# Performance work log

Measured on AMD Instinct MI355X. Metric: run time of the kernel, lower is better.

Reference implementation:

```python
import jax, jax.numpy as jnp
import numpy as np

SCALING = 32.0 / 16.0  # lora_alpha / lora_rank


def setup_inputs() -> dict:
    key = jax.random.key(0)
    ks = jax.random.split(key, 6)
    B_, S, D, O, E, R = 4, 2048, 4096, 4096, 8, 16
    x = jax.random.normal(ks[0], (B_, S, D), dtype=jnp.float32)
    W_base = jax.random.normal(ks[1], (O, D), dtype=jnp.float32) * (D ** -0.5)
    b_base = jax.random.normal(ks[2], (O,), dtype=jnp.float32) * 0.01
    W_gate = jax.random.normal(ks[3], (E, D), dtype=jnp.float32) * (D ** -0.5)
    A = jax.random.normal(ks[4], (E, R, D), dtype=jnp.float32) * (D ** -0.5)
    B = jax.random.normal(ks[5], (O, R), dtype=jnp.float32)[None] * (R ** -0.5)
    B = jnp.broadcast_to(B, (E, O, R)) * jnp.linspace(0.5, 1.5, E)[:, None, None]
    return {"x": x, "W_base": W_base, "b_base": b_base, "W_gate": W_gate,
            "A": A, "B": B, "top_k": 2}


def reference(x, W_base, b_base, W_gate, A, B, top_k):
    D = x.shape[-1]
    O = W_base.shape[0]
    E = W_gate.shape[0]
    xf = x.reshape(-1, D)                      # [N, D] flattened tokens
    N = xf.shape[0]

    # base linear
    base = jnp.einsum('nd,od->no', xf, W_base) + b_base          # [N, O]

    # gating: softmax then top-k, renormalize selected weights
    gate_logits = jax.nn.softmax(xf @ W_gate.T, axis=-1)          # [N, E]
    w, sel = jax.lax.top_k(gate_logits, top_k)                    # [N, k]
    w = w / jnp.sum(w, axis=-1, keepdims=True)

    # dense per-(token, expert) weight; non-selected experts get 0,
    # equivalent to the scatter-add combine in the original code.
    w_dense = jnp.zeros((N, E), dtype=x.dtype).at[
        jnp.arange(N)[:, None], sel].set(w)                       # [N, E]

    # LoRA expert compute: down-proj for every expert (rank is small),
    # weight, then up-proj and combine across experts.
    h = jnp.einsum('nd,erd->ner', xf, A)                          # [N, E, R]
    hw = h * w_dense[:, :, None]                                  # [N, E, R]
    moe = jnp.einsum('ner,eor->no', hw, B) * SCALING              # [N, O]

    out = (base + moe).reshape(x.shape[:-1] + (O,))
    return out
```

## Files before the change

kernel.cpp:

```cpp
#include <hip/hip_runtime.h>
#include <stdint.h>

typedef unsigned short u16;
typedef float f32x4 __attribute__((ext_vector_type(4)));
typedef short bf16x8 __attribute__((ext_vector_type(8)));

static __device__ __forceinline__ u16 f2bf(float f) {
  union { float f; unsigned u; } a; a.f = f;
  unsigned r = a.u + 0x7fffu + ((a.u >> 16) & 1u);
  return (u16)(r >> 16);
}

static __device__ __forceinline__ void gld16(const void* g, void* l) {
  __builtin_amdgcn_global_load_lds(
      (const __attribute__((address_space(1))) void*)(uintptr_t)g,
      (__attribute__((address_space(3))) void*)(uintptr_t)l,
      16, 0, 0);
}

__global__ __launch_bounds__(256) void cast_strided(
    const float* __restrict__ src, u16* __restrict__ dst,
    int rows, int cols, int ldd) {
  const size_t total = (size_t)rows * cols / 4;
  for (size_t i = (size_t)blockIdx.x * 256 + threadIdx.x; i < total;
       i += (size_t)gridDim.x * 256) {
    const size_t e = i * 4;
    const int r = (int)(e / cols);
    const int c = (int)(e % cols);
    float4 v = *(const float4*)(src + e);
    ushort4 o;
    o.x = f2bf(v.x); o.y = f2bf(v.y); o.z = f2bf(v.z); o.w = f2bf(v.w);
    *(ushort4*)(dst + (size_t)r * ldd + c) = o;
  }
}

__global__ __launch_bounds__(256) void cast_b2(
    const float* __restrict__ B, u16* __restrict__ Waug) {
  int i = blockIdx.x * 256 + threadIdx.x;
  if (i >= 4096 * 128) return;
  const int o = i >> 7;
  const int er = i & 127;
  const int e = er >> 4;
  const int r = er & 15;
  float v = B[((size_t)e * 4096 + o) * 16 + r] * 2.0f;
  Waug[(size_t)o * 4224 + 4096 + er] = f2bf(v);
}

__global__ __launch_bounds__(256) void cast_x_gate(
    const float* __restrict__ x, const float* __restrict__ Wg,
    u16* __restrict__ Xaug, float* __restrict__ wsc) {
  const int lane = threadIdx.x & 63;
  const int wv = threadIdx.x >> 6;
  const int n = blockIdx.x * 4 + wv;
  const float4* x4 = (const float4*)(x + (size_t)n * 4096);
  const float4* g4 = (const float4*)Wg;
  u16* xr = Xaug + (size_t)n * 4224;
  float acc[8] = {0, 0, 0, 0, 0, 0, 0, 0};
#pragma unroll
  for (int ii = 0; ii < 16; ++ii) {
    const int i = ii * 64 + lane;
    float4 xv = x4[i];
    ushort4 o;
    o.x = f2bf(xv.x); o.y = f2bf(xv.y); o.z = f2bf(xv.z); o.w = f2bf(xv.w);
    *(ushort4*)(xr + i * 4) = o;
#pragma unroll
    for (int e = 0; e < 8; ++e) {
      float4 w4 = g4[e * 1024 + i];
      acc[e] += xv.x * w4.x + xv.y * w4.y + xv.z * w4.z + xv.w * w4.w;
    }
  }
#pragma unroll
  for (int e = 0; e < 8; ++e) {
#pragma unroll
    for (int off = 32; off > 0; off >>= 1)
      acc[e] += __shfl_xor(acc[e], off);
  }
  int i1 = 0; float m1 = acc[0];
#pragma unroll
  for (int e = 1; e < 8; ++e) if (acc[e] > m1) { m1 = acc[e]; i1 = e; }
  int i2 = -1; float m2 = -3.4e38f;
#pragma unroll
  for (int e = 0; e < 8; ++e) if (e != i1 && acc[e] > m2) { m2 = acc[e]; i2 = e; }
  float w1 = 1.0f / (1.0f + expf(m2 - m1));
  float w2 = 1.0f - w1;
  if (lane < 8)
    wsc[(size_t)n * 8 + lane] = (lane == i1) ? w1 : ((lane == i2) ? w2 : 0.0f);
}

__global__ __launch_bounds__(256) void lora_down(
    const u16* __restrict__ Xa, const u16* __restrict__ A2,
    float* __restrict__ hp) {
  __shared__ u16 sA[128 * 64];
  __shared__ u16 sB[128 * 64];
  const int t = threadIdx.x;
  const int lane = t & 63;
  const int wr = t >> 7;
  const int wc = (t >> 6) & 1;
  const int l15 = lane & 15;
  const int lhi = lane >> 4;
  f32x4 acc[4][4] = {};

  const int brow = blockIdx.x * 128;
  const int kbase = blockIdx.y * 1024;
  const int srow = t >> 3;
  const int scol = (t & 7) * 8;
  const size_t a_src = (size_t)(brow + srow) * 4224 + scol + kbase;
  const size_t b_src = (size_t)srow * 4096 + scol + kbase;

  for (int k0 = 0; k0 < 1024; k0 += 64) {
#pragma unroll
    for (int c = 0; c < 4; ++c)
      gld16(Xa + a_src + (size_t)c * 32 * 4224 + k0,
            &sA[(c * 32 + srow) * 64 + scol]);
#pragma unroll
    for (int c = 0; c < 4; ++c)
      gld16(A2 + b_src + (size_t)c * 32 * 4096 + k0,
            &sB[(c * 32 + srow) * 64 + scol]);
    __syncthreads();
#pragma unroll
    for (int kk = 0; kk < 2; ++kk) {
      bf16x8 av[4], bv[4];
#pragma unroll
      for (int m = 0; m < 4; ++m)
        av[m] = *(const bf16x8*)&sA[(wr * 64 + m * 16 + l15) * 64 + kk * 32 + lhi * 8];
#pragma unroll
      for (int n = 0; n < 4; ++n)
        bv[n] = *(const bf16x8*)&sB[(wc * 64 + n * 16 + l15) * 64 + kk * 32 + lhi * 8];
#pragma unroll
      for (int m = 0; m < 4; ++m)
#pragma unroll
        for (int n = 0; n < 4; ++n)
          acc[m][n] = __builtin_amdgcn_mfma_f32_16x16x32_bf16(av[m], bv[n], acc[m][n], 0, 0, 0);
    }
    __syncthreads();
  }
  float* out = hp + (size_t)blockIdx.y * (8192 * 128);
#pragma unroll
  for (int m = 0; m < 4; ++m) {
    const int rbase = brow + wr * 64 + m * 16 + lhi * 4;
#pragma unroll
    for (int n = 0; n < 4; ++n) {
      const int col = wc * 64 + n * 16 + l15;
#pragma unroll
      for (int j = 0; j < 4; ++j)
        out[(size_t)(rbase + j) * 128 + col] = acc[m][n][j];
    }
  }
}

__global__ __launch_bounds__(256) void reduce_hw(
    const float* __restrict__ hp, const float* __restrict__ wsc,
    u16* __restrict__ Xaug) {
  int i = blockIdx.x * 256 + threadIdx.x;
  if (i >= 8192 * 128) return;
  const int n = i >> 7;
  const int er = i & 127;
  const int e = er >> 4;
  float v = hp[i] + hp[i + 1048576] + hp[i + 2097152] + hp[i + 3145728];
  Xaug[(size_t)n * 4224 + 4096 + er] = f2bf(v * wsc[n * 8 + e]);
}

#define BAR do { asm volatile("" ::: "memory"); __builtin_amdgcn_s_barrier(); asm volatile("" ::: "memory"); } while (0)

#define RDA(BUF, MH)                                                            \
  { _Pragma("unroll") for (int mm = 0; mm < 4; ++mm)                            \
    _Pragma("unroll") for (int kk = 0; kk < 2; ++kk)                            \
      av[mm][kk] = *(const bf16x8*)(lds + (BUF) + fbA + ((((MH) * 4 + mm) * 2 + kk) << 10)); }

#define RDB(BUF, NH)                                                            \
  { _Pragma("unroll") for (int nn = 0; nn < 2; ++nn)                            \
    _Pragma("unroll") for (int kk = 0; kk < 2; ++kk)                            \
      bv[(NH) * 2 + nn][kk] = *(const bf16x8*)(lds + (BUF) + fbB + ((((NH) * 2 + nn) * 2 + kk) << 10)); }

#define MFMAQ(MH, NH)                                                           \
  { __builtin_amdgcn_s_setprio(1);                                              \
    _Pragma("unroll") for (int kk = 0; kk < 2; ++kk)                            \
    _Pragma("unroll") for (int mm = 0; mm < 4; ++mm)                            \
    _Pragma("unroll") for (int nn = 0; nn < 2; ++nn)                            \
      acc[(MH) * 4 + mm][(NH) * 2 + nn] = __builtin_amdgcn_mfma_f32_16x16x32_bf16( \
          av[mm][kk], bv[(NH) * 2 + nn][kk], acc[(MH) * 4 + mm][(NH) * 2 + nn], 0, 0, 0); \
    __builtin_amdgcn_s_setprio(0); }

__global__ __launch_bounds__(512, 2) void gemm8p(
    const u16* __restrict__ Ag, const u16* __restrict__ Bg,
    const float* __restrict__ bias, float* __restrict__ C,
    int lda, int ldb, int ldc, int K, int tiles_n) {
  __shared__ __align__(1024) char lds[131072];
  const int t = threadIdx.x;
  const int lane = t & 63;
  const int w = t >> 6;
  const int wr = w >> 2, wc = w & 3;
  const int l15 = lane & 15, lhi = lane >> 4;

  const int cpx = gridDim.x >> 3;
  const int bid = blockIdx.x;
  const int swz = (bid & 7) * cpx + (bid >> 3);
  const int tile_m = swz / tiles_n;
  const int tile_n = swz % tiles_n;
  const int brow = tile_m << 8;
  const int bcol = tile_n << 8;

  const int sb = (lane << 4) ^ (lane & 32);
  const int srow = sb >> 6;
  const int scol = (sb & 63) >> 1;

  const u16* pA[4]; const u16* pB[4];
#pragma unroll
  for (int s = 0; s < 4; ++s) {
    const int idx = w * 4 + s;
    const int rg = idx >> 1, cs = idx & 1;
    pA[s] = Ag + (size_t)(brow + rg * 16 + srow) * lda + cs * 32 + scol;
    pB[s] = Bg + (size_t)(bcol + rg * 16 + srow) * ldb + cs * 32 + scol;
  }
  const int ldsA = w << 12;
  const int ldsB = 32768 + (w << 12);

  const int innerL = ((l15 << 6) + (lhi << 4)) ^ ((l15 & 8) << 2);
  const int fbA = (wr << 14) + innerL;
  const int fbB = 32768 + (wc << 13) + innerL;

  f32x4 acc[8][4] = {};
  bf16x8 av[4][2], bv[4][2];

  const int NT = K >> 6;

#pragma unroll
  for (int s = 0; s < 4; ++s) gld16(pA[s], lds + ldsA + (s << 10));
#pragma unroll
  for (int s = 0; s < 4; ++s) gld16(pB[s], lds + ldsB + (s << 10));
#pragma unroll
  for (int s = 0; s < 4; ++s) gld16(pB[s] + 64, lds + 65536 + ldsB + (s << 10));
#pragma unroll
  for (int s = 0; s < 4; ++s) { pA[s] += 64; pB[s] += 128; }
  asm volatile("s_waitcnt vmcnt(4)" ::: "memory");
  BAR;
  RDA(0, 0); RDB(0, 0);

  for (int j = 0; j < NT; ++j) {
    const int buf  = (j & 1) << 16;
    const int obuf = buf ^ 65536;
    const bool stA = (j + 1 < NT);
    const bool stB = (j + 2 < NT);
    if (stA) { gld16(pA[0], lds + obuf + ldsA);
               gld16(pA[1], lds + obuf + ldsA + 1024); }
    MFMAQ(0, 0);
    RDB(buf, 1);
    BAR;
    if (stA) { gld16(pA[2], lds + obuf + ldsA + 2048);
               gld16(pA[3], lds + obuf + ldsA + 3072); }
    MFMAQ(0, 1);
    RDA(buf, 1);
    BAR;
    if (stB) { gld16(pB[0], lds + buf + ldsB);
               gld16(pB[1], lds + buf + ldsB + 1024); }
    MFMAQ(1, 1);
    BAR;
    if (stB) { gld16(pB[2], lds + buf + ldsB + 2048);
               gld16(pB[3], lds + buf + ldsB + 3072); }
    if (j < NT - 2)       { asm volatile("s_waitcnt vmcnt(4)" ::: "memory"); }
    else if (j == NT - 2) { asm volatile("s_waitcnt vmcnt(0)" ::: "memory"); }
    BAR;
    MFMAQ(1, 0);
    if (stA) { RDA(obuf, 0); RDB(obuf, 0); }
#pragma unroll
    for (int s = 0; s < 4; ++s) { pA[s] += 64; pB[s] += 64; }
  }

#pragma unroll
  for (int m = 0; m < 8; ++m) {
    const int row0 = brow + wr * 128 + m * 16 + lhi * 4;
#pragma unroll
    for (int n = 0; n < 4; ++n) {
      const int col = bcol + wc * 64 + n * 16 + l15;
      const float b2 = bias[col];
#pragma unroll
      for (int j = 0; j < 4; ++j)
        C[(size_t)(row0 + j) * ldc + col] = acc[m][n][j] + b2;
    }
  }
}

extern "C" void kernel_launch(void* const* d_in, const int* in_sizes, int n_in,
                              void* d_out, int out_size, void* d_ws, size_t ws_size,
                              hipStream_t stream) {
  const float* x  = (const float*)d_in[0];
  const float* Wb = (const float*)d_in[1];
  const float* bb = (const float*)d_in[2];
  const float* Wg = (const float*)d_in[3];
  const float* A  = (const float*)d_in[4];
  const float* B  = (const float*)d_in[5];
  float* out = (float*)d_out;

  char* ws = (char*)d_ws;
  u16*   Xaug = (u16*)ws;
  u16*   Waug = (u16*)(ws + 69206016);
  u16*   a2   = (u16*)(ws + 69206016 + 34603008);
  float* wsc  = (float*)(ws + 69206016 + 34603008 + 1048576);
  float* hp   = out;

  cast_x_gate<<<2048, 256, 0, stream>>>(x, Wg, Xaug, wsc);

  cast_strided<<<2048, 256, 0, stream>>>(Wb, Waug, 4096, 4096, 4224);
  cast_strided<<<512,  256, 0, stream>>>(A,  a2,   128,  4096, 4096);
  cast_b2<<<2048, 256, 0, stream>>>(B, Waug);

  lora_down<<<dim3(64, 4), 256, 0, stream>>>(Xaug, a2, hp);

  reduce_hw<<<4096, 256, 0, stream>>>(hp, wsc, Xaug);

  gemm8p<<<512, 512, 0, stream>>>(Xaug, Waug, bb, out, 4224, 4224, 4096, 4224, 16);
}
```

Baseline: 391.9 us.

## Switch main GEMM to 32x32x16 MFMA tiles and reorder block-to-tile mapping

Replaces the 16x16x32 bf16 MFMA fragments with 32x32x16 fragments. This changes the LDS read addressing (with an XOR swizzle bit), the register accumulator layout and the epilogue store pattern. The larger MFMA shape halves the number of matrix instructions and LDS fragment reads per wave. The block-to-tile mapping is also changed to a fixed grouping that makes neighbouring blocks share A row tiles, aiming at better L2 reuse. The mapping is now hardcoded for a 32x16 tile grid, and the 32-wide column store pattern may coalesce differently.

```diff
diff --git a/kernel.cpp b/kernel.cpp
--- a/kernel.cpp
+++ b/kernel.cpp
@@ -3,6 +3,7 @@
 
 typedef unsigned short u16;
 typedef float f32x4 __attribute__((ext_vector_type(4)));
+typedef float f32x16 __attribute__((ext_vector_type(16)));
 typedef short bf16x8 __attribute__((ext_vector_type(8)));
 
 static __device__ __forceinline__ u16 f2bf(float f) {
@@ -162,41 +163,39 @@
 
 #define BAR do { asm volatile("" ::: "memory"); __builtin_amdgcn_s_barrier(); asm volatile("" ::: "memory"); } while (0)
 
-#define RDA(BUF, MH)                                                            \
-  { _Pragma("unroll") for (int mm = 0; mm < 4; ++mm)                            \
-    _Pragma("unroll") for (int kk = 0; kk < 2; ++kk)                            \
-      av[mm][kk] = *(const bf16x8*)(lds + (BUF) + fbA + ((((MH) * 4 + mm) * 2 + kk) << 10)); }
-
-#define RDB(BUF, NH)                                                            \
-  { _Pragma("unroll") for (int nn = 0; nn < 2; ++nn)                            \
-    _Pragma("unroll") for (int kk = 0; kk < 2; ++kk)                            \
-      bv[(NH) * 2 + nn][kk] = *(const bf16x8*)(lds + (BUF) + fbB + ((((NH) * 2 + nn) * 2 + kk) << 10)); }
-
-#define MFMAQ(MH, NH)                                                           \
-  { __builtin_amdgcn_s_setprio(1);                                              \
-    _Pragma("unroll") for (int kk = 0; kk < 2; ++kk)                            \
-    _Pragma("unroll") for (int mm = 0; mm < 4; ++mm)                            \
-    _Pragma("unroll") for (int nn = 0; nn < 2; ++nn)                            \
-      acc[(MH) * 4 + mm][(NH) * 2 + nn] = __builtin_amdgcn_mfma_f32_16x16x32_bf16( \
-          av[mm][kk], bv[(NH) * 2 + nn][kk], acc[(MH) * 4 + mm][(NH) * 2 + nn], 0, 0, 0); \
+#define RDA32(BUF, MH)                                                           \
+  { _Pragma("unroll") for (int m2 = 0; m2 < 2; ++m2)                             \
+    _Pragma("unroll") for (int kk = 0; kk < 4; ++kk)                             \
+      av[m2][kk] = *(const bf16x8*)(lds + (BUF) + fA + ((((MH) * 2 + m2)) << 12) \
+                     + ((kk >> 1) << 10) + ((((kk & 1) ^ sbit)) << 5)); }
+
+#define RDB32(BUF, NH)                                                           \
+  { _Pragma("unroll") for (int kk = 0; kk < 4; ++kk)                             \
+      bv[NH][kk] = *(const bf16x8*)(lds + (BUF) + fB + ((NH) << 12)              \
+                     + ((kk >> 1) << 10) + ((((kk & 1) ^ sbit)) << 5)); }
+
+#define MFMAQ32(MH, NH)                                                          \
+  { __builtin_amdgcn_s_setprio(1);                                               \
+    _Pragma("unroll") for (int kk = 0; kk < 4; ++kk)                             \
+    _Pragma("unroll") for (int m2 = 0; m2 < 2; ++m2)                             \
+      acc[(MH) * 2 + m2][NH] = __builtin_amdgcn_mfma_f32_32x32x16_bf16(          \
+          av[m2][kk], bv[NH][kk], acc[(MH) * 2 + m2][NH], 0, 0, 0);              \
     __builtin_amdgcn_s_setprio(0); }
 
 __global__ __launch_bounds__(512, 2) void gemm8p(
     const u16* __restrict__ Ag, const u16* __restrict__ Bg,
     const float* __restrict__ bias, float* __restrict__ C,
-    int lda, int ldb, int ldc, int K, int tiles_n) {
+    int lda, int ldb, int ldc, int K) {
   __shared__ __align__(1024) char lds[131072];
   const int t = threadIdx.x;
   const int lane = t & 63;
   const int w = t >> 6;
   const int wr = w >> 2, wc = w & 3;
-  const int l15 = lane & 15, lhi = lane >> 4;
-
-  const int cpx = gridDim.x >> 3;
+
   const int bid = blockIdx.x;
-  const int swz = (bid & 7) * cpx + (bid >> 3);
-  const int tile_m = swz / tiles_n;
-  const int tile_n = swz % tiles_n;
+  const int g = bid >> 3;
+  const int tile_m = (bid & 7) * 4 + (g & 3);
+  const int tile_n = g >> 2;
   const int brow = tile_m << 8;
   const int bcol = tile_n << 8;
 
@@ -215,12 +214,15 @@
   const int ldsA = w << 12;
   const int ldsB = 32768 + (w << 12);
 
-  const int innerL = ((l15 << 6) + (lhi << 4)) ^ ((l15 & 8) << 2);
-  const int fbA = (wr << 14) + innerL;
-  const int fbB = 32768 + (wc << 13) + innerL;
-
-  f32x4 acc[8][4] = {};
-  bf16x8 av[4][2], bv[4][2];
+  const int r = lane & 31;
+  const int khalf = lane >> 5;
+  const int sbit = (r >> 3) & 1;
+  const int fin = ((r & 15) << 6) + (khalf << 4);
+  const int fA = (wr << 14) + ((r >> 4) << 11) + fin;
+  const int fB = 32768 + (wc << 13) + ((r >> 4) << 11) + fin;
+
+  f32x16 acc[4][2] = {};
+  bf16x8 av[2][4], bv[2][4];
 
   const int NT = K >> 6;
 
@@ -234,7 +236,7 @@
   for (int s = 0; s < 4; ++s) { pA[s] += 64; pB[s] += 128; }
   asm volatile("s_waitcnt vmcnt(4)" ::: "memory");
   BAR;
-  RDA(0, 0); RDB(0, 0);
+  RDA32(0, 0); RDB32(0, 0);
 
   for (int j = 0; j < NT; ++j) {
     const int buf  = (j & 1) << 16;
@@ -243,39 +245,41 @@
     const bool stB = (j + 2 < NT);
     if (stA) { gld16(pA[0], lds + obuf + ldsA);
                gld16(pA[1], lds + obuf + ldsA + 1024); }
-    MFMAQ(0, 0);
-    RDB(buf, 1);
+    MFMAQ32(0, 0);
+    RDB32(buf, 1);
     BAR;
     if (stA) { gld16(pA[2], lds + obuf + ldsA + 2048);
                gld16(pA[3], lds + obuf + ldsA + 3072); }
-    MFMAQ(0, 1);
-    RDA(buf, 1);
+    MFMAQ32(0, 1);
+    RDA32(buf, 1);
     BAR;
     if (stB) { gld16(pB[0], lds + buf + ldsB);
                gld16(pB[1], lds + buf + ldsB + 1024); }
-    MFMAQ(1, 1);
+    MFMAQ32(1, 1);
     BAR;
     if (stB) { gld16(pB[2], lds + buf + ldsB + 2048);
                gld16(pB[3], lds + buf + ldsB + 3072); }
     if (j < NT - 2)       { asm volatile("s_waitcnt vmcnt(4)" ::: "memory"); }
     else if (j == NT - 2) { asm volatile("s_waitcnt vmcnt(0)" ::: "memory"); }
     BAR;
-    MFMAQ(1, 0);
-    if (stA) { RDA(obuf, 0); RDB(obuf, 0); }
+    MFMAQ32(1, 0);
+    if (stA) { RDA32(obuf, 0); RDB32(obuf, 0); }
 #pragma unroll
     for (int s = 0; s < 4; ++s) { pA[s] += 64; pB[s] += 64; }
   }
 
 #pragma unroll
-  for (int m = 0; m < 8; ++m) {
-    const int row0 = brow + wr * 128 + m * 16 + lhi * 4;
-#pragma unroll
-    for (int n = 0; n < 4; ++n) {
-      const int col = bcol + wc * 64 + n * 16 + l15;
+  for (int mm = 0; mm < 4; ++mm) {
+    const int rowb = brow + wr * 128 + mm * 32 + 4 * khalf;
+#pragma unroll
+    for (int nn = 0; nn < 2; ++nn) {
+      const int col = bcol + wc * 64 + nn * 32 + r;
       const float b2 = bias[col];
 #pragma unroll
-      for (int j = 0; j < 4; ++j)
-        C[(size_t)(row0 + j) * ldc + col] = acc[m][n][j] + b2;
+      for (int reg = 0; reg < 16; ++reg) {
+        const int row = rowb + (reg & 3) + 8 * (reg >> 2);
+        C[(size_t)row * ldc + col] = acc[mm][nn][reg] + b2;
+      }
     }
   }
 }
@@ -308,5 +312,5 @@
 
   reduce_hw<<<4096, 256, 0, stream>>>(hp, wsc, Xaug);
 
-  gemm8p<<<512, 512, 0, stream>>>(Xaug, Waug, bb, out, 4224, 4224, 4096, 4224, 16);
-}
+  gemm8p<<<512, 512, 0, stream>>>(Xaug, Waug, bb, out, 4224, 4224, 4096, 4224);
+}
```

Result: slower. 423.1 us (+8.0%).

## Triple-buffer B tiles in GEMM, cut barriers, and fuse weight cast kernels

Applied to the files above, without the earlier changes.

The main GEMM now uses 160KB of LDS: double-buffered A tiles and triple-buffered B tiles. Loads for a whole tile are issued at the start of each iteration, so only one wait and barrier is needed per K-step instead of four, which removes synchronisation stalls between the MFMA phases. The block-to-tile mapping is changed to a fixed grouping that favours L2 reuse. The W_base and LoRA-B bf16 casts are merged into a single kernel to save a launch and a strided pass. The larger LDS footprint caps occupancy, and the looser barrier placement depends on the vmcnt accounting being correct.

```diff
diff --git a/kernel.cpp b/kernel.cpp
--- a/kernel.cpp
+++ b/kernel.cpp
@@ -16,6 +16,31 @@
       (const __attribute__((address_space(1))) void*)(uintptr_t)g,
       (__attribute__((address_space(3))) void*)(uintptr_t)l,
       16, 0, 0);
+}
+
+__global__ __launch_bounds__(256) void cast_w(
+    const float* __restrict__ Wb, const float* __restrict__ B,
+    u16* __restrict__ Waug) {
+  const int total = 4096 * 1056;
+  for (int v = blockIdx.x * 256 + threadIdx.x; v < total;
+       v += gridDim.x * 256) {
+    const int o = v / 1056;
+    const int cv = v - o * 1056;
+    const int c = cv * 4;
+    ushort4 out;
+    if (c < 4096) {
+      float4 w = *(const float4*)(Wb + (size_t)o * 4096 + c);
+      out.x = f2bf(w.x); out.y = f2bf(w.y); out.z = f2bf(w.z); out.w = f2bf(w.w);
+    } else {
+      const int er = c - 4096;
+      const int e = er >> 4;
+      const int r = er & 15;
+      const float* bp = B + ((size_t)e * 4096 + o) * 16 + r;
+      out.x = f2bf(bp[0] * 2.0f); out.y = f2bf(bp[1] * 2.0f);
+      out.z = f2bf(bp[2] * 2.0f); out.w = f2bf(bp[3] * 2.0f);
+    }
+    *(ushort4*)(Waug + (size_t)o * 4224 + c) = out;
+  }
 }
 
 __global__ __launch_bounds__(256) void cast_strided(
@@ -34,18 +59,6 @@
   }
 }
 
-__global__ __launch_bounds__(256) void cast_b2(
-    const float* __restrict__ B, u16* __restrict__ Waug) {
-  int i = blockIdx.x * 256 + threadIdx.x;
-  if (i >= 4096 * 128) return;
-  const int o = i >> 7;
-  const int er = i & 127;
-  const int e = er >> 4;
-  const int r = er & 15;
-  float v = B[((size_t)e * 4096 + o) * 16 + r] * 2.0f;
-  Waug[(size_t)o * 4224 + 4096 + er] = f2bf(v);
-}
-
 __global__ __launch_bounds__(256) void cast_x_gate(
     const float* __restrict__ x, const float* __restrict__ Wg,
     u16* __restrict__ Xaug, float* __restrict__ wsc) {
@@ -184,19 +197,18 @@
 __global__ __launch_bounds__(512, 2) void gemm8p(
     const u16* __restrict__ Ag, const u16* __restrict__ Bg,
     const float* __restrict__ bias, float* __restrict__ C,
-    int lda, int ldb, int ldc, int K, int tiles_n) {
-  __shared__ __align__(1024) char lds[131072];
+    int lda, int ldb, int ldc, int K) {
+  __shared__ __align__(1024) char lds[163840];
   const int t = threadIdx.x;
   const int lane = t & 63;
   const int w = t >> 6;
   const int wr = w >> 2, wc = w & 3;
   const int l15 = lane & 15, lhi = lane >> 4;
 
-  const int cpx = gridDim.x >> 3;
   const int bid = blockIdx.x;
-  const int swz = (bid & 7) * cpx + (bid >> 3);
-  const int tile_m = swz / tiles_n;
-  const int tile_n = swz % tiles_n;
+  const int g = bid >> 3;
+  const int tile_m = (bid & 7) * 4 + (g & 3);
+  const int tile_n = g >> 2;
   const int brow = tile_m << 8;
   const int bcol = tile_n << 8;
 
@@ -212,12 +224,11 @@
     pA[s] = Ag + (size_t)(brow + rg * 16 + srow) * lda + cs * 32 + scol;
     pB[s] = Bg + (size_t)(bcol + rg * 16 + srow) * ldb + cs * 32 + scol;
   }
-  const int ldsA = w << 12;
-  const int ldsB = 32768 + (w << 12);
+  const int ldsW = w << 12;
 
   const int innerL = ((l15 << 6) + (lhi << 4)) ^ ((l15 & 8) << 2);
   const int fbA = (wr << 14) + innerL;
-  const int fbB = 32768 + (wc << 13) + innerL;
+  const int fbB = (wc << 13) + innerL;
 
   f32x4 acc[8][4] = {};
   bf16x8 av[4][2], bv[4][2];
@@ -225,43 +236,48 @@
   const int NT = K >> 6;
 
 #pragma unroll
-  for (int s = 0; s < 4; ++s) gld16(pA[s], lds + ldsA + (s << 10));
-#pragma unroll
-  for (int s = 0; s < 4; ++s) gld16(pB[s], lds + ldsB + (s << 10));
-#pragma unroll
-  for (int s = 0; s < 4; ++s) gld16(pB[s] + 64, lds + 65536 + ldsB + (s << 10));
+  for (int s = 0; s < 4; ++s) gld16(pA[s],       lds + (s << 10) + ldsW);
+#pragma unroll
+  for (int s = 0; s < 4; ++s) gld16(pB[s],       lds + 65536 + (s << 10) + ldsW);
+#pragma unroll
+  for (int s = 0; s < 4; ++s) gld16(pA[s] + 64,  lds + 32768 + (s << 10) + ldsW);
+#pragma unroll
+  for (int s = 0; s < 4; ++s) gld16(pB[s] + 64,  lds + 98304 + (s << 10) + ldsW);
+#pragma unroll
+  for (int s = 0; s < 4; ++s) gld16(pB[s] + 128, lds + 131072 + (s << 10) + ldsW);
 #pragma unroll
   for (int s = 0; s < 4; ++s) { pA[s] += 64; pB[s] += 128; }
-  asm volatile("s_waitcnt vmcnt(4)" ::: "memory");
+  asm volatile("s_waitcnt vmcnt(12)" ::: "memory");
   BAR;
-  RDA(0, 0); RDB(0, 0);
+
+  int bA = 0;
+  int bB = 65536;
+  int bB2 = 131072;
 
   for (int j = 0; j < NT; ++j) {
-    const int buf  = (j & 1) << 16;
-    const int obuf = buf ^ 65536;
-    const bool stA = (j + 1 < NT);
-    const bool stB = (j + 2 < NT);
-    if (stA) { gld16(pA[0], lds + obuf + ldsA);
-               gld16(pA[1], lds + obuf + ldsA + 1024); }
+    const int obA = bA ^ 32768;
+    const bool stA = (j >= 1) & (j + 1 < NT);
+    const bool stB = (j >= 1) & (j + 2 < NT);
+    RDA(bA, 0); RDB(bB, 0);
+    if (stA) {
+#pragma unroll
+      for (int s = 0; s < 4; ++s) gld16(pA[s], lds + obA + (s << 10) + ldsW);
+    }
+    if (stB) {
+#pragma unroll
+      for (int s = 0; s < 4; ++s) gld16(pB[s], lds + bB2 + (s << 10) + ldsW);
+    }
     MFMAQ(0, 0);
-    RDB(buf, 1);
-    BAR;
-    if (stA) { gld16(pA[2], lds + obuf + ldsA + 2048);
-               gld16(pA[3], lds + obuf + ldsA + 3072); }
+    RDB(bB, 1);
     MFMAQ(0, 1);
-    RDA(buf, 1);
-    BAR;
-    if (stB) { gld16(pB[0], lds + buf + ldsB);
-               gld16(pB[1], lds + buf + ldsB + 1024); }
+    RDA(bA, 1);
     MFMAQ(1, 1);
-    BAR;
-    if (stB) { gld16(pB[2], lds + buf + ldsB + 2048);
-               gld16(pB[3], lds + buf + ldsB + 3072); }
-    if (j < NT - 2)       { asm volatile("s_waitcnt vmcnt(4)" ::: "memory"); }
-    else if (j == NT - 2) { asm volatile("s_waitcnt vmcnt(0)" ::: "memory"); }
-    BAR;
     MFMAQ(1, 0);
-    if (stA) { RDA(obuf, 0); RDB(obuf, 0); }
+    if (j < NT - 2)       { asm volatile("s_waitcnt vmcnt(4)" ::: "memory"); BAR; }
+    else if (j == NT - 2) { asm volatile("s_waitcnt vmcnt(0)" ::: "memory"); BAR; }
+    bA = obA;
+    bB = (bB == 131072) ? 65536 : bB + 32768;
+    bB2 = (bB2 == 131072) ? 65536 : bB2 + 32768;
 #pragma unroll
     for (int s = 0; s < 4; ++s) { pA[s] += 64; pB[s] += 64; }
   }
@@ -274,8 +290,8 @@
       const int col = bcol + wc * 64 + n * 16 + l15;
       const float b2 = bias[col];
 #pragma unroll
-      for (int j = 0; j < 4; ++j)
-        C[(size_t)(row0 + j) * ldc + col] = acc[m][n][j] + b2;
+      for (int jj = 0; jj < 4; ++jj)
+        C[(size_t)(row0 + jj) * ldc + col] = acc[m][n][jj] + b2;
     }
   }
 }
@@ -300,13 +316,12 @@
 
   cast_x_gate<<<2048, 256, 0, stream>>>(x, Wg, Xaug, wsc);
 
-  cast_strided<<<2048, 256, 0, stream>>>(Wb, Waug, 4096, 4096, 4224);
-  cast_strided<<<512,  256, 0, stream>>>(A,  a2,   128,  4096, 4096);
-  cast_b2<<<2048, 256, 0, stream>>>(B, Waug);
+  cast_w<<<2048, 256, 0, stream>>>(Wb, B, Waug);
+  cast_strided<<<512, 256, 0, stream>>>(A, a2, 128, 4096, 4096);
 
   lora_down<<<dim3(64, 4), 256, 0, stream>>>(Xaug, a2, hp);
 
   reduce_hw<<<4096, 256, 0, stream>>>(hp, wsc, Xaug);
 
-  gemm8p<<<512, 512, 0, stream>>>(Xaug, Waug, bb, out, 4224, 4224, 4096, 4224, 16);
-}
+  gemm8p<<<512, 512, 0, stream>>>(Xaug, Waug, bb, out, 4224, 4224, 4096, 4224);
+}
```

Result: no change. 396.5 us (+1.2%).

## Fuse preprocessing casts into one kernel and fold LoRA reduce into down-proj

Applied to the files above, without the earlier changes.

Merges the x cast plus gating, the W_base/B cast and the A cast into a single multi-role kernel launch. The LoRA down-projection is restructured from a 4-way split-K with a separate fp32 reduce pass into one full-K kernel of 32-row tiles that applies the gate weights and writes bf16 directly into the augmented X buffer. The GEMM tile-to-block mapping is also reworked to a fixed grouped swizzle. This removes several launches and the fp32 partial-sum round trip through memory, but the new down-proj kernel has only 256 small blocks over a long K loop with no double buffering, which may leave it underused.

```diff
diff --git a/kernel.cpp b/kernel.cpp
--- a/kernel.cpp
+++ b/kernel.cpp
@@ -18,146 +18,147 @@
       16, 0, 0);
 }
 
-__global__ __launch_bounds__(256) void cast_strided(
-    const float* __restrict__ src, u16* __restrict__ dst,
-    int rows, int cols, int ldd) {
-  const size_t total = (size_t)rows * cols / 4;
-  for (size_t i = (size_t)blockIdx.x * 256 + threadIdx.x; i < total;
-       i += (size_t)gridDim.x * 256) {
-    const size_t e = i * 4;
-    const int r = (int)(e / cols);
-    const int c = (int)(e % cols);
-    float4 v = *(const float4*)(src + e);
+__global__ __launch_bounds__(256) void fused_pre(
+    const float* __restrict__ x, const float* __restrict__ Wg,
+    const float* __restrict__ Wb, const float* __restrict__ B,
+    const float* __restrict__ A,
+    u16* __restrict__ Xaug, u16* __restrict__ Waug, u16* __restrict__ a2,
+    float* __restrict__ wsc) {
+  const int bid = blockIdx.x;
+  const int t = threadIdx.x;
+  if (bid < 2048) {
+    const int lane = t & 63;
+    const int wv = t >> 6;
+    const int n = bid * 4 + wv;
+    const float4* x4 = (const float4*)(x + (size_t)n * 4096);
+    const float4* g4 = (const float4*)Wg;
+    u16* xr = Xaug + (size_t)n * 4224;
+    float acc[8] = {0, 0, 0, 0, 0, 0, 0, 0};
+#pragma unroll
+    for (int ii = 0; ii < 16; ++ii) {
+      const int i = ii * 64 + lane;
+      float4 xv = x4[i];
+      ushort4 o;
+      o.x = f2bf(xv.x); o.y = f2bf(xv.y); o.z = f2bf(xv.z); o.w = f2bf(xv.w);
+      *(ushort4*)(xr + i * 4) = o;
+#pragma unroll
+      for (int e = 0; e < 8; ++e) {
+        float4 w4 = g4[e * 1024 + i];
+        acc[e] += xv.x * w4.x + xv.y * w4.y + xv.z * w4.z + xv.w * w4.w;
+      }
+    }
+#pragma unroll
+    for (int e = 0; e < 8; ++e) {
+#pragma unroll
+      for (int off = 32; off > 0; off >>= 1)
+        acc[e] += __shfl_xor(acc[e], off);
+    }
+    int i1 = 0; float m1 = acc[0];
+#pragma unroll
+    for (int e = 1; e < 8; ++e) if (acc[e] > m1) { m1 = acc[e]; i1 = e; }
+    int i2 = -1; float m2 = -3.4e38f;
+#pragma unroll
+    for (int e = 0; e < 8; ++e) if (e != i1 && acc[e] > m2) { m2 = acc[e]; i2 = e; }
+    float w1 = 1.0f / (1.0f + expf(m2 - m1));
+    float w2 = 1.0f - w1;
+    if (lane < 8)
+      wsc[(size_t)n * 8 + lane] = (lane == i1) ? w1 : ((lane == i2) ? w2 : 0.0f);
+  } else if (bid < 4096) {
+    const int total = 4096 * 1056;
+    for (int v = (bid - 2048) * 256 + t; v < total; v += 2048 * 256) {
+      const int o = v / 1056;
+      const int c = (v - o * 1056) * 4;
+      ushort4 out;
+      if (c < 4096) {
+        float4 w = *(const float4*)(Wb + (size_t)o * 4096 + c);
+        out.x = f2bf(w.x); out.y = f2bf(w.y); out.z = f2bf(w.z); out.w = f2bf(w.w);
+      } else {
+        const int er = c - 4096;
+        const int e = er >> 4;
+        const int r = er & 15;
+        const float* bp = B + ((size_t)e * 4096 + o) * 16 + r;
+        out.x = f2bf(bp[0] * 2.0f); out.y = f2bf(bp[1] * 2.0f);
+        out.z = f2bf(bp[2] * 2.0f); out.w = f2bf(bp[3] * 2.0f);
+      }
+      *(ushort4*)(Waug + (size_t)o * 4224 + c) = out;
+    }
+  } else {
+    const int i = (bid - 4096) * 256 + t;
+    const size_t e = (size_t)i * 4;
+    float4 v = *(const float4*)(A + e);
     ushort4 o;
     o.x = f2bf(v.x); o.y = f2bf(v.y); o.z = f2bf(v.z); o.w = f2bf(v.w);
-    *(ushort4*)(dst + (size_t)r * ldd + c) = o;
-  }
-}
-
-__global__ __launch_bounds__(256) void cast_b2(
-    const float* __restrict__ B, u16* __restrict__ Waug) {
-  int i = blockIdx.x * 256 + threadIdx.x;
-  if (i >= 4096 * 128) return;
-  const int o = i >> 7;
-  const int er = i & 127;
-  const int e = er >> 4;
-  const int r = er & 15;
-  float v = B[((size_t)e * 4096 + o) * 16 + r] * 2.0f;
-  Waug[(size_t)o * 4224 + 4096 + er] = f2bf(v);
-}
-
-__global__ __launch_bounds__(256) void cast_x_gate(
-    const float* __restrict__ x, const float* __restrict__ Wg,
-    u16* __restrict__ Xaug, float* __restrict__ wsc) {
-  const int lane = threadIdx.x & 63;
-  const int wv = threadIdx.x >> 6;
-  const int n = blockIdx.x * 4 + wv;
-  const float4* x4 = (const float4*)(x + (size_t)n * 4096);
-  const float4* g4 = (const float4*)Wg;
-  u16* xr = Xaug + (size_t)n * 4224;
-  float acc[8] = {0, 0, 0, 0, 0, 0, 0, 0};
-#pragma unroll
-  for (int ii = 0; ii < 16; ++ii) {
-    const int i = ii * 64 + lane;
-    float4 xv = x4[i];
-    ushort4 o;
-    o.x = f2bf(xv.x); o.y = f2bf(xv.y); o.z = f2bf(xv.z); o.w = f2bf(xv.w);
-    *(ushort4*)(xr + i * 4) = o;
-#pragma unroll
-    for (int e = 0; e < 8; ++e) {
-      float4 w4 = g4[e * 1024 + i];
-      acc[e] += xv.x * w4.x + xv.y * w4.y + xv.z * w4.z + xv.w * w4.w;
-    }
-  }
-#pragma unroll
-  for (int e = 0; e < 8; ++e) {
-#pragma unroll
-    for (int off = 32; off > 0; off >>= 1)
-      acc[e] += __shfl_xor(acc[e], off);
-  }
-  int i1 = 0; float m1 = acc[0];
-#pragma unroll
-  for (int e = 1; e < 8; ++e) if (acc[e] > m1) { m1 = acc[e]; i1 = e; }
-  int i2 = -1; float m2 = -3.4e38f;
-#pragma unroll
-  for (int e = 0; e < 8; ++e) if (e != i1 && acc[e] > m2) { m2 = acc[e]; i2 = e; }
-  float w1 = 1.0f / (1.0f + expf(m2 - m1));
-  float w2 = 1.0f - w1;
-  if (lane < 8)
-    wsc[(size_t)n * 8 + lane] = (lane == i1) ? w1 : ((lane == i2) ? w2 : 0.0f);
-}
-
-__global__ __launch_bounds__(256) void lora_down(
+    *(ushort4*)(a2 + e) = o;
+  }
+}
+
+__global__ __launch_bounds__(256) void lora_hw(
     const u16* __restrict__ Xa, const u16* __restrict__ A2,
-    float* __restrict__ hp) {
-  __shared__ u16 sA[128 * 64];
-  __shared__ u16 sB[128 * 64];
+    const float* __restrict__ wsc, u16* __restrict__ Xaug) {
+  __shared__ __align__(1024) char lds[20480];
   const int t = threadIdx.x;
   const int lane = t & 63;
-  const int wr = t >> 7;
-  const int wc = (t >> 6) & 1;
-  const int l15 = lane & 15;
-  const int lhi = lane >> 4;
-  f32x4 acc[4][4] = {};
-
-  const int brow = blockIdx.x * 128;
-  const int kbase = blockIdx.y * 1024;
-  const int srow = t >> 3;
-  const int scol = (t & 7) * 8;
-  const size_t a_src = (size_t)(brow + srow) * 4224 + scol + kbase;
-  const size_t b_src = (size_t)srow * 4096 + scol + kbase;
-
-  for (int k0 = 0; k0 < 1024; k0 += 64) {
-#pragma unroll
-    for (int c = 0; c < 4; ++c)
-      gld16(Xa + a_src + (size_t)c * 32 * 4224 + k0,
-            &sA[(c * 32 + srow) * 64 + scol]);
-#pragma unroll
-    for (int c = 0; c < 4; ++c)
-      gld16(A2 + b_src + (size_t)c * 32 * 4096 + k0,
-            &sB[(c * 32 + srow) * 64 + scol]);
+  const int w = t >> 6;
+  const int l15 = lane & 15, lhi = lane >> 4;
+  const int brow = blockIdx.x * 32;
+
+  const int sb = (lane << 4) ^ (lane & 32);
+  const int srow = sb >> 6;
+  const int scol = (sb & 63) >> 1;
+
+  const u16* pA = Xa + (size_t)(brow + (w >> 1) * 16 + srow) * 4224 + (w & 1) * 32 + scol;
+  const u16* pB[4];
+#pragma unroll
+  for (int s = 0; s < 4; ++s) {
+    const int idx = w * 4 + s;
+    pB[s] = A2 + (size_t)((idx >> 1) * 16 + srow) * 4096 + (idx & 1) * 32 + scol;
+  }
+  const int dA = w << 10;
+  const int dB = 4096 + (w << 12);
+
+  const int innerL = ((l15 << 6) + (lhi << 4)) ^ ((l15 & 8) << 2);
+
+  f32x4 acc[2][2] = {};
+
+  for (int k0 = 0; k0 < 4096; k0 += 64) {
+    gld16(pA + k0, lds + dA);
+#pragma unroll
+    for (int s = 0; s < 4; ++s) gld16(pB[s] + k0, lds + dB + (s << 10));
     __syncthreads();
-#pragma unroll
-    for (int kk = 0; kk < 2; ++kk) {
-      bf16x8 av[4], bv[4];
-#pragma unroll
-      for (int m = 0; m < 4; ++m)
-        av[m] = *(const bf16x8*)&sA[(wr * 64 + m * 16 + l15) * 64 + kk * 32 + lhi * 8];
-#pragma unroll
-      for (int n = 0; n < 4; ++n)
-        bv[n] = *(const bf16x8*)&sB[(wc * 64 + n * 16 + l15) * 64 + kk * 32 + lhi * 8];
-#pragma unroll
-      for (int m = 0; m < 4; ++m)
-#pragma unroll
-        for (int n = 0; n < 4; ++n)
-          acc[m][n] = __builtin_amdgcn_mfma_f32_16x16x32_bf16(av[m], bv[n], acc[m][n], 0, 0, 0);
-    }
+    bf16x8 av[2][2], bv[2][2];
+#pragma unroll
+    for (int m = 0; m < 2; ++m)
+#pragma unroll
+      for (int kk = 0; kk < 2; ++kk)
+        av[m][kk] = *(const bf16x8*)(lds + ((m * 2 + kk) << 10) + innerL);
+#pragma unroll
+    for (int n = 0; n < 2; ++n)
+#pragma unroll
+      for (int kk = 0; kk < 2; ++kk)
+        bv[n][kk] = *(const bf16x8*)(lds + 4096 + (((w * 2 + n) * 2 + kk) << 10) + innerL);
+#pragma unroll
+    for (int kk = 0; kk < 2; ++kk)
+#pragma unroll
+      for (int m = 0; m < 2; ++m)
+#pragma unroll
+        for (int n = 0; n < 2; ++n)
+          acc[m][n] = __builtin_amdgcn_mfma_f32_16x16x32_bf16(av[m][kk], bv[n][kk], acc[m][n], 0, 0, 0);
     __syncthreads();
   }
-  float* out = hp + (size_t)blockIdx.y * (8192 * 128);
-#pragma unroll
-  for (int m = 0; m < 4; ++m) {
-    const int rbase = brow + wr * 64 + m * 16 + lhi * 4;
-#pragma unroll
-    for (int n = 0; n < 4; ++n) {
-      const int col = wc * 64 + n * 16 + l15;
-#pragma unroll
-      for (int j = 0; j < 4; ++j)
-        out[(size_t)(rbase + j) * 128 + col] = acc[m][n][j];
-    }
-  }
-}
-
-__global__ __launch_bounds__(256) void reduce_hw(
-    const float* __restrict__ hp, const float* __restrict__ wsc,
-    u16* __restrict__ Xaug) {
-  int i = blockIdx.x * 256 + threadIdx.x;
-  if (i >= 8192 * 128) return;
-  const int n = i >> 7;
-  const int er = i & 127;
-  const int e = er >> 4;
-  float v = hp[i] + hp[i + 1048576] + hp[i + 2097152] + hp[i + 3145728];
-  Xaug[(size_t)n * 4224 + 4096 + er] = f2bf(v * wsc[n * 8 + e]);
+#pragma unroll
+  for (int m = 0; m < 2; ++m) {
+    const int rbase = brow + m * 16 + lhi * 4;
+#pragma unroll
+    for (int n = 0; n < 2; ++n) {
+      const int col = w * 32 + n * 16 + l15;
+#pragma unroll
+      for (int j = 0; j < 4; ++j) {
+        const int row = rbase + j;
+        const float g = wsc[(size_t)row * 8 + (col >> 4)];
+        Xaug[(size_t)row * 4224 + 4096 + col] = f2bf(acc[m][n][j] * g);
+      }
+    }
+  }
 }
 
 #define BAR do { asm volatile("" ::: "memory"); __builtin_amdgcn_s_barrier(); asm volatile("" ::: "memory"); } while (0)
@@ -184,7 +185,7 @@
 __global__ __launch_bounds__(512, 2) void gemm8p(
     const u16* __restrict__ Ag, const u16* __restrict__ Bg,
     const float* __restrict__ bias, float* __restrict__ C,
-    int lda, int ldb, int ldc, int K, int tiles_n) {
+    int lda, int ldb, int ldc, int K) {
   __shared__ __align__(1024) char lds[131072];
   const int t = threadIdx.x;
   const int lane = t & 63;
@@ -192,11 +193,10 @@
   const int wr = w >> 2, wc = w & 3;
   const int l15 = lane & 15, lhi = lane >> 4;
 
-  const int cpx = gridDim.x >> 3;
   const int bid = blockIdx.x;
-  const int swz = (bid & 7) * cpx + (bid >> 3);
-  const int tile_m = swz / tiles_n;
-  const int tile_n = swz % tiles_n;
+  const int g = bid >> 3;
+  const int tile_m = (bid & 7) * 4 + (g & 3);
+  const int tile_n = g >> 2;
   const int brow = tile_m << 8;
   const int bcol = tile_n << 8;
 
@@ -274,8 +274,8 @@
       const int col = bcol + wc * 64 + n * 16 + l15;
       const float b2 = bias[col];
 #pragma unroll
-      for (int j = 0; j < 4; ++j)
-        C[(size_t)(row0 + j) * ldc + col] = acc[m][n][j] + b2;
+      for (int jj = 0; jj < 4; ++jj)
+        C[(size_t)(row0 + jj) * ldc + col] = acc[m][n][jj] + b2;
     }
   }
 }
@@ -296,17 +296,10 @@
   u16*   Waug = (u16*)(ws + 69206016);
   u16*   a2   = (u16*)(ws + 69206016 + 34603008);
   float* wsc  = (float*)(ws + 69206016 + 34603008 + 1048576);
-  float* hp   = out;
-
-  cast_x_gate<<<2048, 256, 0, stream>>>(x, Wg, Xaug, wsc);
-
-  cast_strided<<<2048, 256, 0, stream>>>(Wb, Waug, 4096, 4096, 4224);
-  cast_strided<<<512,  256, 0, stream>>>(A,  a2,   128,  4096, 4096);
-  cast_b2<<<2048, 256, 0, stream>>>(B, Waug);
-
-  lora_down<<<dim3(64, 4), 256, 0, stream>>>(Xaug, a2, hp);
-
-  reduce_hw<<<4096, 256, 0, stream>>>(hp, wsc, Xaug);
-
-  gemm8p<<<512, 512, 0, stream>>>(Xaug, Waug, bb, out, 4224, 4224, 4096, 4224, 16);
-}
+
+  fused_pre<<<4608, 256, 0, stream>>>(x, Wg, Wb, B, A, Xaug, Waug, a2, wsc);
+
+  lora_hw<<<256, 256, 0, stream>>>(Xaug, a2, wsc, Xaug);
+
+  gemm8p<<<512, 512, 0, stream>>>(Xaug, Waug, bb, out, 4224, 4224, 4096, 4224);
+}
```

New measurement: 385.4 us. Within noise of the previous version (-1.7%).
